# Performance work log

Hardware: AMD Instinct MI355X
Metric: run time of the kernel (lower is better)

Reference implementation:

```python
import jax, jax.numpy as jnp
import numpy as np

IN_DIM, OUT_DIM = 256, 64
ALPHA = 0.2  # leaky relu negative slope
NEG_INF = -1e30


def setup_inputs() -> dict:
    key = jax.random.key(0)
    k1, k2, k3, k4 = jax.random.split(key, 4)
    B, N = 8, 2048
    h = jax.random.normal(k1, (B, N, IN_DIM), dtype=jnp.float32)
    adj = jax.random.randint(k2, (B, N, N), 0, 2, dtype=jnp.int32)
    # ensure no fully-isolated node (avoids softmax over all -inf)
    idx = jnp.arange(N)
    adj = adj.at[:, idx, idx].set(1)
    # params: fc.weight [out,in] -> store transposed [in,out]; attn_fc.weight [1, 2*out] -> [2*out]
    W = jax.random.normal(k3, (IN_DIM, OUT_DIM), dtype=jnp.float32) / np.sqrt(IN_DIM)
    a = jax.random.normal(k4, (2 * OUT_DIM,), dtype=jnp.float32) / np.sqrt(2 * OUT_DIM)
    return {"h": h, "adj": adj, "W": W, "a": a}


def reference(h, adj, W, a):
    # Wh: [B,N,D]
    Wh = jnp.einsum("bni,io->bno", h, W)
    D = Wh.shape[-1]
    # concat-based additive attention decomposed: e[b,i,j] = lrelu(a1.Wh_i + a2.Wh_j)
    a1, a2 = a[:D], a[D:]
    s1 = Wh @ a1  # [B,N] contribution of row node i
    s2 = Wh @ a2  # [B,N] contribution of col node j
    e = jax.nn.leaky_relu(s1[:, :, None] + s2[:, None, :], negative_slope=ALPHA)  # [B,N,N]
    e = jnp.where(adj == 0, NEG_INF, e)
    attn = jax.nn.softmax(e, axis=-1)
    # dropout is identity in eval mode
    return jnp.einsum("bij,bjd->bid", attn, Wh)
```

## Files before the change

### kernel.cpp

```cpp
#include <hip/hip_runtime.h>
#include <math.h>

#define NB 8
#define NN 2048
#define IN_DIM 256
#define OUT_DIM 64
#define ALPHA 0.2f
#define JSPLIT 4
#define PACK_BLOCKS (NB * NN * NN / 32 / 256)
#define WH_BLOCKS 256

typedef __attribute__((ext_vector_type(8))) short bf16x8;
typedef __attribute__((ext_vector_type(4))) float f32x4;
typedef __attribute__((ext_vector_type(4))) int   i32x4;

__device__ __forceinline__ unsigned short f2bf(float x) {
    union { float f; unsigned u; } v; v.f = x;
    unsigned r = v.u + 0x7FFF + ((v.u >> 16) & 1);
    return (unsigned short)(r >> 16);
}

#define WT_STRIDE 264
__global__ __launch_bounds__(256) void prep_kernel(const float* __restrict__ h,
                                                   const float* __restrict__ W,
                                                   const float* __restrict__ a,
                                                   const int* __restrict__ adj,
                                                   unsigned* __restrict__ bits,
                                                   unsigned short* __restrict__ Whbt,
                                                   float* __restrict__ s1,
                                                   float* __restrict__ s2) {
    __shared__ unsigned short Wt[OUT_DIM * WT_STRIDE];
    const int t = threadIdx.x;
    const int bid = blockIdx.x;

    if (bid >= WH_BLOCKS) {
        const long w = (long)(bid - WH_BLOCKS) * 256 + t;
        const i32x4* a4 = (const i32x4*)adj + w * 8;
        unsigned mm = 0;
        #pragma unroll
        for (int q = 0; q < 8; ++q) {
            const i32x4 v = __builtin_nontemporal_load(a4 + q);
            mm |= (v.x != 0 ? 1u : 0u) << (4 * q);
            mm |= (v.y != 0 ? 1u : 0u) << (4 * q + 1);
            mm |= (v.z != 0 ? 1u : 0u) << (4 * q + 2);
            mm |= (v.w != 0 ? 1u : 0u) << (4 * q + 3);
        }
        bits[w] = mm;
        return;
    }

    #pragma unroll 8
    for (int rep = 0; rep < 64; ++rep) {
        const int id = rep * 256 + t;
        const int k = id >> 6, n = id & 63;
        Wt[n * WT_STRIDE + k] = f2bf(W[id]);
    }
    __syncthreads();

    const int lane = t & 63, wv = t >> 6;
    const int m = lane & 15, quad = lane >> 4;
    const long gr0 = (long)(bid * 4 + wv) * 16;

    f32x4 acc[4];
    #pragma unroll
    for (int nt = 0; nt < 4; ++nt) acc[nt] = (f32x4){0.f, 0.f, 0.f, 0.f};

    #pragma unroll
    for (int ks = 0; ks < 8; ++ks) {
        const int k0 = ks * 32;
        const float* hp = h + (gr0 + m) * IN_DIM + k0 + quad * 8;
        const float4 ha = *(const float4*)hp;
        const float4 hb = *(const float4*)(hp + 4);
        bf16x8 af;
        af[0] = (short)f2bf(ha.x); af[1] = (short)f2bf(ha.y);
        af[2] = (short)f2bf(ha.z); af[3] = (short)f2bf(ha.w);
        af[4] = (short)f2bf(hb.x); af[5] = (short)f2bf(hb.y);
        af[6] = (short)f2bf(hb.z); af[7] = (short)f2bf(hb.w);
        #pragma unroll
        for (int nt = 0; nt < 4; ++nt) {
            const bf16x8 bf_ = *(const bf16x8*)(const void*)
                &Wt[(nt * 16 + m) * WT_STRIDE + k0 + quad * 8];
            acc[nt] = __builtin_amdgcn_mfma_f32_16x16x32_bf16(af, bf_, acc[nt], 0, 0, 0);
        }
    }

    const int b  = (int)(gr0 >> 11);
    const int ib = (int)(gr0 & 2047);

    #pragma unroll
    for (int nt = 0; nt < 4; ++nt) {
        ushort4 w4;
        w4.x = f2bf(acc[nt][0]); w4.y = f2bf(acc[nt][1]);
        w4.z = f2bf(acc[nt][2]); w4.w = f2bf(acc[nt][3]);
        *(ushort4*)&Whbt[((long)(b * OUT_DIM + nt * 16 + m) << 11) + ib + quad * 4] = w4;
    }

    float a1v[4], a2v[4];
    #pragma unroll
    for (int nt = 0; nt < 4; ++nt) {
        a1v[nt] = a[nt * 16 + m];
        a2v[nt] = a[OUT_DIM + nt * 16 + m];
    }
    #pragma unroll
    for (int reg = 0; reg < 4; ++reg) {
        float p1 = 0.f, p2 = 0.f;
        #pragma unroll
        for (int nt = 0; nt < 4; ++nt) {
            p1 += acc[nt][reg] * a1v[nt];
            p2 += acc[nt][reg] * a2v[nt];
        }
        #pragma unroll
        for (int off = 1; off < 16; off <<= 1) {
            p1 += __shfl_xor(p1, off, 64);
            p2 += __shfl_xor(p2, off, 64);
        }
        if (m == 0) {
            s1[gr0 + quad * 4 + reg] = p1;
            s2[gr0 + quad * 4 + reg] = p2;
        }
    }
}

__device__ __forceinline__ float pcalc(unsigned mask, int bit, float s2e, float s1v) {
    float e = s1v + s2e;
    e = e > 0.f ? e : ALPHA * e;
    const float p = __expf(e);
    return ((mask >> bit) & 1u) ? p : 0.f;
}

__global__ __launch_bounds__(256, 4) void attn_kernel(const unsigned* __restrict__ bits,
                                                      const unsigned short* __restrict__ Whbt,
                                                      const float* __restrict__ s1,
                                                      const float* __restrict__ s2,
                                                      float* __restrict__ part,
                                                      float* __restrict__ lpart) {
    const int t = threadIdx.x, lane = t & 63, wv = t >> 6;
    const int bid = blockIdx.x;
    const int js  = bid & (JSPLIT - 1);
    const int itg = (bid >> 2) & 31;
    const int b   = bid >> 7;
    const int i0  = itg * 64 + wv * 16;
    const int jlo = js * (NN / JSPLIT);

    const int m = lane & 15, quad = lane >> 4;

    const i32x4* mp = (const i32x4*)(bits + ((long)(b * NN + i0 + m) << 6) + (jlo >> 5));
    i32x4 mk[4];
    #pragma unroll
    for (int g = 0; g < 4; ++g) mk[g] = mp[g];

    const float* s2p  = s2 + b * NN + jlo + quad * 8;
    const unsigned short* wbase = Whbt + ((long)(b * OUT_DIM) << 11) + jlo + quad * 8;
    const float s1v = s1[b * NN + i0 + m];

    f32x4 acc[4];
    #pragma unroll
    for (int nt = 0; nt < 4; ++nt) acc[nt] = (f32x4){0.f, 0.f, 0.f, 0.f};
    f32x4 racc = (f32x4){0.f, 0.f, 0.f, 0.f};

    bf16x8 bones;
    #pragma unroll
    for (int e = 0; e < 8; ++e) bones[e] = (short)0x3F80;

    float4 sv0 = *(const float4*)s2p;
    float4 sv1 = *(const float4*)(s2p + 4);

    #pragma unroll
    for (int ks = 0; ks < 16; ++ks) {
        const int j0 = ks * 32;
        const unsigned mask = (unsigned)mk[ks >> 2][ks & 3];

        bf16x8 bfr[4];
        #pragma unroll
        for (int nt = 0; nt < 4; ++nt)
            bfr[nt] = *(const bf16x8*)(const void*)
                &wbase[(((long)(nt * 16 + m)) << 11) + j0];

        const float4 cs0 = sv0, cs1 = sv1;
        if (ks < 15) {
            sv0 = *(const float4*)(s2p + j0 + 32);
            sv1 = *(const float4*)(s2p + j0 + 36);
        }

        const int bb = quad * 8;
        float pv[8];
        pv[0] = pcalc(mask, bb + 0, cs0.x, s1v);
        pv[1] = pcalc(mask, bb + 1, cs0.y, s1v);
        pv[2] = pcalc(mask, bb + 2, cs0.z, s1v);
        pv[3] = pcalc(mask, bb + 3, cs0.w, s1v);
        pv[4] = pcalc(mask, bb + 4, cs1.x, s1v);
        pv[5] = pcalc(mask, bb + 5, cs1.y, s1v);
        pv[6] = pcalc(mask, bb + 6, cs1.z, s1v);
        pv[7] = pcalc(mask, bb + 7, cs1.w, s1v);

        bf16x8 af;
        #pragma unroll
        for (int e = 0; e < 8; ++e) af[e] = (short)f2bf(pv[e]);

        #pragma unroll
        for (int nt = 0; nt < 4; ++nt)
            acc[nt] = __builtin_amdgcn_mfma_f32_16x16x32_bf16(af, bfr[nt], acc[nt], 0, 0, 0);
        racc = __builtin_amdgcn_mfma_f32_16x16x32_bf16(af, bones, racc, 0, 0, 0);
    }

    if (m == 0) {
        #pragma unroll
        for (int reg = 0; reg < 4; ++reg)
            lpart[js * (NB * NN) + b * NN + i0 + quad * 4 + reg] = racc[reg];
    }

    float* pp = part + (long)js * ((long)NB * NN * OUT_DIM)
                     + ((long)(b * NN + i0) << 6);
    #pragma unroll
    for (int nt = 0; nt < 4; ++nt)
        #pragma unroll
        for (int reg = 0; reg < 4; ++reg)
            pp[(quad * 4 + reg) * OUT_DIM + nt * 16 + m] = acc[nt][reg];
}

__global__ __launch_bounds__(256) void finalize_kernel(const float* __restrict__ part,
                                                       const float* __restrict__ lpart,
                                                       float* __restrict__ out) {
    const int idx = blockIdx.x * 256 + threadIdx.x;
    const int row = idx >> 4;
    float l = 0.f;
    #pragma unroll
    for (int s = 0; s < JSPLIT; ++s) l += lpart[s * (NB * NN) + row];
    float4 v = make_float4(0.f, 0.f, 0.f, 0.f);
    const float4* p4 = (const float4*)part;
    #pragma unroll
    for (int s = 0; s < JSPLIT; ++s) {
        const float4 p = p4[(long)s * ((long)NB * NN * OUT_DIM / 4) + idx];
        v.x += p.x; v.y += p.y; v.z += p.z; v.w += p.w;
    }
    const float inv = 1.f / l;
    v.x *= inv; v.y *= inv; v.z *= inv; v.w *= inv;
    ((float4*)out)[idx] = v;
}

extern "C" void kernel_launch(void* const* d_in, const int* in_sizes, int n_in,
                              void* d_out, int out_size, void* d_ws, size_t ws_size,
                              hipStream_t stream) {
    const float* h   = (const float*)d_in[0];
    const int*   adj = (const int*)d_in[1];
    const float* W   = (const float*)d_in[2];
    const float* a   = (const float*)d_in[3];
    float* out = (float*)d_out;

    float* s1    = (float*)d_ws;
    float* s2    = s1 + NB * NN;
    float* lpart = s2 + NB * NN;
    float* part  = lpart + JSPLIT * NB * NN;
    unsigned short* Whbt =
        (unsigned short*)(part + (long)JSPLIT * NB * NN * OUT_DIM);
    unsigned* bits = (unsigned*)(Whbt + (long)NB * NN * OUT_DIM);

    prep_kernel<<<WH_BLOCKS + PACK_BLOCKS, 256, 0, stream>>>(h, W, a, adj, bits,
                                                             Whbt, s1, s2);
    attn_kernel<<<NB * (NN / 64) * JSPLIT, 256, 0, stream>>>(bits, Whbt, s1, s2,
                                                             part, lpart);
    finalize_kernel<<<NB * NN * OUT_DIM / 4 / 256, 256, 0, stream>>>(part, lpart, out);
}
```

Before: 269.2 us.

## Fuse split-K reduction into attention kernel and pack adjacency with wave ballot

Each attention block now covers 16 rows, and its four waves each handle a quarter of the columns. The partial sums are reduced through shared memory and normalized in-kernel, which removes the finalize kernel and the global partial buffers. Adjacency packing now uses a wave-wide ballot on coalesced 64-int loads to build 64-bit masks instead of per-thread bit assembly. The changes cut the global writes and reads of partials and one launch, at the cost of a block-level sync and a partly unrolled inner loop.

```diff
diff --git a/kernel.cpp b/kernel.cpp
--- a/kernel.cpp
+++ b/kernel.cpp
@@ -6,9 +6,8 @@
 #define IN_DIM 256
 #define OUT_DIM 64
 #define ALPHA 0.2f
-#define JSPLIT 4
-#define PACK_BLOCKS (NB * NN * NN / 32 / 256)
 #define WH_BLOCKS 256
+#define PACK_BLOCKS 4096
 
 typedef __attribute__((ext_vector_type(8))) short bf16x8;
 typedef __attribute__((ext_vector_type(4))) float f32x4;
@@ -25,7 +24,7 @@
                                                    const float* __restrict__ W,
                                                    const float* __restrict__ a,
                                                    const int* __restrict__ adj,
-                                                   unsigned* __restrict__ bits,
+                                                   unsigned long long* __restrict__ bits64,
                                                    unsigned short* __restrict__ Whbt,
                                                    float* __restrict__ s1,
                                                    float* __restrict__ s2) {
@@ -34,18 +33,16 @@
     const int bid = blockIdx.x;
 
     if (bid >= WH_BLOCKS) {
-        const long w = (long)(bid - WH_BLOCKS) * 256 + t;
-        const i32x4* a4 = (const i32x4*)adj + w * 8;
-        unsigned mm = 0;
-        #pragma unroll
-        for (int q = 0; q < 8; ++q) {
-            const i32x4 v = __builtin_nontemporal_load(a4 + q);
-            mm |= (v.x != 0 ? 1u : 0u) << (4 * q);
-            mm |= (v.y != 0 ? 1u : 0u) << (4 * q + 1);
-            mm |= (v.z != 0 ? 1u : 0u) << (4 * q + 2);
-            mm |= (v.w != 0 ? 1u : 0u) << (4 * q + 3);
-        }
-        bits[w] = mm;
+        const int lane = t & 63;
+        const int wg = (bid - WH_BLOCKS) * 4 + (t >> 6);
+        const long base = (long)wg * 32;
+        const int* ap = adj + base * 64 + lane;
+        #pragma unroll 4
+        for (int it = 0; it < 32; ++it) {
+            const int v = __builtin_nontemporal_load(ap + it * 64);
+            const unsigned long long mk = __ballot(v != 0);
+            if (lane == 0) bits64[base + it] = mk;
+        }
         return;
     }
 
@@ -128,28 +125,28 @@
     return ((mask >> bit) & 1u) ? p : 0.f;
 }
 
-__global__ __launch_bounds__(256, 4) void attn_kernel(const unsigned* __restrict__ bits,
+__global__ __launch_bounds__(256, 4) void attn_kernel(const unsigned long long* __restrict__ bits64,
                                                       const unsigned short* __restrict__ Whbt,
                                                       const float* __restrict__ s1,
                                                       const float* __restrict__ s2,
-                                                      float* __restrict__ part,
-                                                      float* __restrict__ lpart) {
+                                                      float* __restrict__ out) {
+    __shared__ float ored[4][16][65];
+    __shared__ float olsum[4][16];
+
     const int t = threadIdx.x, lane = t & 63, wv = t >> 6;
     const int bid = blockIdx.x;
-    const int js  = bid & (JSPLIT - 1);
-    const int itg = (bid >> 2) & 31;
     const int b   = bid >> 7;
-    const int i0  = itg * 64 + wv * 16;
-    const int jlo = js * (NN / JSPLIT);
+    const int i0  = (bid & 127) * 16;
+    const int jlo = wv * (NN / 4);
 
     const int m = lane & 15, quad = lane >> 4;
 
-    const i32x4* mp = (const i32x4*)(bits + ((long)(b * NN + i0 + m) << 6) + (jlo >> 5));
-    i32x4 mk[4];
-    #pragma unroll
-    for (int g = 0; g < 4; ++g) mk[g] = mp[g];
-
-    const float* s2p  = s2 + b * NN + jlo + quad * 8;
+    const i32x4* mp = (const i32x4*)bits64 + ((long)(b * NN + i0 + m) << 4) + (wv << 2);
+    i32x4 mku[4];
+    #pragma unroll
+    for (int g = 0; g < 4; ++g) mku[g] = mp[g];
+
+    const float* s2p = s2 + b * NN + jlo + quad * 8;
     const unsigned short* wbase = Whbt + ((long)(b * OUT_DIM) << 11) + jlo + quad * 8;
     const float s1v = s1[b * NN + i0 + m];
 
@@ -165,10 +162,10 @@
     float4 sv0 = *(const float4*)s2p;
     float4 sv1 = *(const float4*)(s2p + 4);
 
-    #pragma unroll
+    #pragma unroll 2
     for (int ks = 0; ks < 16; ++ks) {
         const int j0 = ks * 32;
-        const unsigned mask = (unsigned)mk[ks >> 2][ks & 3];
+        const unsigned mask = (unsigned)mku[ks >> 2][ks & 3];
 
         bf16x8 bfr[4];
         #pragma unroll
@@ -203,39 +200,29 @@
         racc = __builtin_amdgcn_mfma_f32_16x16x32_bf16(af, bones, racc, 0, 0, 0);
     }
 
+    #pragma unroll
+    for (int nt = 0; nt < 4; ++nt)
+        #pragma unroll
+        for (int reg = 0; reg < 4; ++reg)
+            ored[wv][quad * 4 + reg][nt * 16 + m] = acc[nt][reg];
     if (m == 0) {
         #pragma unroll
         for (int reg = 0; reg < 4; ++reg)
-            lpart[js * (NB * NN) + b * NN + i0 + quad * 4 + reg] = racc[reg];
-    }
-
-    float* pp = part + (long)js * ((long)NB * NN * OUT_DIM)
-                     + ((long)(b * NN + i0) << 6);
-    #pragma unroll
-    for (int nt = 0; nt < 4; ++nt)
-        #pragma unroll
-        for (int reg = 0; reg < 4; ++reg)
-            pp[(quad * 4 + reg) * OUT_DIM + nt * 16 + m] = acc[nt][reg];
-}
-
-__global__ __launch_bounds__(256) void finalize_kernel(const float* __restrict__ part,
-                                                       const float* __restrict__ lpart,
-                                                       float* __restrict__ out) {
-    const int idx = blockIdx.x * 256 + threadIdx.x;
-    const int row = idx >> 4;
-    float l = 0.f;
-    #pragma unroll
-    for (int s = 0; s < JSPLIT; ++s) l += lpart[s * (NB * NN) + row];
-    float4 v = make_float4(0.f, 0.f, 0.f, 0.f);
-    const float4* p4 = (const float4*)part;
-    #pragma unroll
-    for (int s = 0; s < JSPLIT; ++s) {
-        const float4 p = p4[(long)s * ((long)NB * NN * OUT_DIM / 4) + idx];
-        v.x += p.x; v.y += p.y; v.z += p.z; v.w += p.w;
-    }
-    const float inv = 1.f / l;
-    v.x *= inv; v.y *= inv; v.z *= inv; v.w *= inv;
-    ((float4*)out)[idx] = v;
+            olsum[wv][quad * 4 + reg] = racc[reg];
+    }
+    __syncthreads();
+
+    const int col = t & 63;
+    const int rb  = t >> 6;
+    float* ob = out + ((long)(b * NN + i0) << 6);
+    #pragma unroll
+    for (int k2 = 0; k2 < 4; ++k2) {
+        const int row = rb + 4 * k2;
+        const float l = olsum[0][row] + olsum[1][row] + olsum[2][row] + olsum[3][row];
+        const float v = ored[0][row][col] + ored[1][row][col]
+                      + ored[2][row][col] + ored[3][row][col];
+        ob[(long)row * OUT_DIM + col] = v / l;
+    }
 }
 
 extern "C" void kernel_launch(void* const* d_in, const int* in_sizes, int n_in,
@@ -247,17 +234,12 @@
     const float* a   = (const float*)d_in[3];
     float* out = (float*)d_out;
 
-    float* s1    = (float*)d_ws;
-    float* s2    = s1 + NB * NN;
-    float* lpart = s2 + NB * NN;
-    float* part  = lpart + JSPLIT * NB * NN;
-    unsigned short* Whbt =
-        (unsigned short*)(part + (long)JSPLIT * NB * NN * OUT_DIM);
-    unsigned* bits = (unsigned*)(Whbt + (long)NB * NN * OUT_DIM);
-
-    prep_kernel<<<WH_BLOCKS + PACK_BLOCKS, 256, 0, stream>>>(h, W, a, adj, bits,
+    unsigned long long* bits64 = (unsigned long long*)d_ws;
+    unsigned short* Whbt = (unsigned short*)(bits64 + NB * NN * NN / 64);
+    float* s1 = (float*)(Whbt + (long)NB * NN * OUT_DIM);
+    float* s2 = s1 + NB * NN;
+
+    prep_kernel<<<WH_BLOCKS + PACK_BLOCKS, 256, 0, stream>>>(h, W, a, adj, bits64,
                                                              Whbt, s1, s2);
-    attn_kernel<<<NB * (NN / 64) * JSPLIT, 256, 0, stream>>>(bits, Whbt, s1, s2,
-                                                             part, lpart);
-    finalize_kernel<<<NB * NN * OUT_DIM / 4 / 256, 256, 0, stream>>>(part, lpart, out);
-}
+    attn_kernel<<<NB * (NN / 16), 256, 0, stream>>>(bits64, Whbt, s1, s2, out);
+}
```

New measurement: 284.4 us. +5.6%, slower.
